# Optimization experiments

Measured on AMD Instinct MI355X. Metric: run time of the kernel, lower is better.

## Reference

```python
import jax, jax.numpy as jnp
import numpy as np

LN_EPS = 1e-5

def _layernorm(x, g, b):
    mu = jnp.mean(x, axis=-1, keepdims=True)
    var = jnp.mean((x - mu) ** 2, axis=-1, keepdims=True)
    return (x - mu) * jax.lax.rsqrt(var + LN_EPS) * g + b

def _mlp(x, w0, b0, wh, bh, lng, lnb, wout, bout):
    # Linear -> ReLU -> LN, repeated; final Linear.
    h = _layernorm(jax.nn.relu(x @ w0.T + b0), lng[0], lnb[0])
    for i in range(wh.shape[0]):
        h = _layernorm(jax.nn.relu(h @ wh[i].T + bh[i]), lng[i + 1], lnb[i + 1])
    return h @ wout.T + bout

def _vq(z, codebook, commitment_cost=0.25):
    B, A, D = z.shape
    flat = z.reshape(-1, D)                                  # [N, D]
    d = (jnp.sum(flat ** 2, axis=1, keepdims=True)
         + jnp.sum(codebook ** 2, axis=1)
         - 2.0 * flat @ codebook.T)                          # [N, K]
    idx = jnp.argmin(d, axis=1)                              # [N]
    quantized = codebook[idx].reshape(z.shape)               # gather, not one-hot matmul
    e_latent = jnp.mean((jax.lax.stop_gradient(quantized) - z) ** 2)
    q_latent = jnp.mean((quantized - jax.lax.stop_gradient(z)) ** 2)
    vq_loss = commitment_cost * e_latent + q_latent
    quantized = z + jax.lax.stop_gradient(quantized - z)     # straight-through
    return quantized, vq_loss

def setup_inputs() -> dict:
    key = jax.random.key(0)
    ks = jax.random.split(key, 8)
    H, D, K = 256, 64, 512
    B, A = 2048, 128
    s = lambda fan_in: 1.0 / np.sqrt(fan_in)
    return {
        'x': jax.random.normal(ks[0], (B, A, 3), jnp.float32),
        'enc_w0': jax.random.normal(ks[1], (H, 3), jnp.float32) * s(3),
        'enc_b0': jnp.zeros((H,), jnp.float32),
        'enc_wh': jax.random.normal(ks[2], (2, H, H), jnp.float32) * s(H),
        'enc_bh': jnp.zeros((2, H), jnp.float32),
        'enc_ln_g': jnp.ones((3, H), jnp.float32),
        'enc_ln_b': jnp.zeros((3, H), jnp.float32),
        'enc_wout': jax.random.normal(ks[3], (D, H), jnp.float32) * s(H),
        'enc_bout': jnp.zeros((D,), jnp.float32),
        'codebook': jax.random.uniform(ks[4], (K, D), jnp.float32, -1.0 / K, 1.0 / K),
        'dec_w0': jax.random.normal(ks[5], (H, D), jnp.float32) * s(D),
        'dec_b0': jnp.zeros((H,), jnp.float32),
        'dec_wh': jax.random.normal(ks[6], (2, H, H), jnp.float32) * s(H),
        'dec_bh': jnp.zeros((2, H), jnp.float32),
        'dec_ln_g': jnp.ones((3, H), jnp.float32),
        'dec_ln_b': jnp.zeros((3, H), jnp.float32),
        'dec_wout': jax.random.normal(ks[7], (3, H), jnp.float32) * s(H),
        'dec_bout': jnp.zeros((3,), jnp.float32),
    }

def reference(x, enc_w0, enc_b0, enc_wh, enc_bh, enc_ln_g, enc_ln_b, enc_wout, enc_bout,
              codebook, dec_w0, dec_b0, dec_wh, dec_bh, dec_ln_g, dec_ln_b, dec_wout, dec_bout):
    z = _mlp(x, enc_w0, enc_b0, enc_wh, enc_bh, enc_ln_g, enc_ln_b, enc_wout, enc_bout)
    quantized, vq_loss = _vq(z, codebook)
    recon = _mlp(quantized, dec_w0, dec_b0, dec_wh, dec_bh, dec_ln_g, dec_ln_b, dec_wout, dec_bout)
    loss = jnp.mean((recon - x) ** 2) + vq_loss
    return recon, quantized, loss
```

## Files before the change

### kernel.cpp

```cpp
#include <hip/hip_runtime.h>
#include <math.h>

__device__ __forceinline__ float fma4(float4 w, float4 a, float acc) {
  return fmaf(w.w, a.w, fmaf(w.z, a.z, fmaf(w.y, a.y, fmaf(w.x, a.x, acc))));
}


template <int NKQ>
__device__ __forceinline__ void gemmW(const float (*A)[256], const float* __restrict__ WT,
                                      float* acc, int r0, int c0) {
  #pragma unroll
  for (int i = 0; i < 32; ++i) acc[i] = 0.f;
  #pragma unroll 1
  for (int kq = 0; kq < NKQ; ++kq) {
    float4 wv[8];
    #pragma unroll
    for (int kk = 0; kk < 4; ++kk) {
      wv[kk * 2]     = *(const float4*)&WT[(size_t)(kq * 4 + kk) * 256 + c0];
      wv[kk * 2 + 1] = *(const float4*)&WT[(size_t)(kq * 4 + kk) * 256 + c0 + 4];
    }
    float4 a_[4];
    #pragma unroll
    for (int i = 0; i < 4; ++i) a_[i] = *(const float4*)&A[r0 + i][kq * 4];
    #pragma unroll
    for (int kk = 0; kk < 4; ++kk) {
      const float4 wlo = wv[kk * 2], whi = wv[kk * 2 + 1];
      #pragma unroll
      for (int i = 0; i < 4; ++i) {
        const float av = kk == 0 ? a_[i].x : kk == 1 ? a_[i].y : kk == 2 ? a_[i].z : a_[i].w;
        acc[i * 8 + 0] = fmaf(av, wlo.x, acc[i * 8 + 0]);
        acc[i * 8 + 1] = fmaf(av, wlo.y, acc[i * 8 + 1]);
        acc[i * 8 + 2] = fmaf(av, wlo.z, acc[i * 8 + 2]);
        acc[i * 8 + 3] = fmaf(av, wlo.w, acc[i * 8 + 3]);
        acc[i * 8 + 4] = fmaf(av, whi.x, acc[i * 8 + 4]);
        acc[i * 8 + 5] = fmaf(av, whi.y, acc[i * 8 + 5]);
        acc[i * 8 + 6] = fmaf(av, whi.z, acc[i * 8 + 6]);
        acc[i * 8 + 7] = fmaf(av, whi.w, acc[i * 8 + 7]);
      }
    }
  }
}

__device__ __forceinline__ void bias_relu(float* acc, const float* __restrict__ Bp, int c0) {
  float bv[8];
  *(float4*)&bv[0] = *(const float4*)&Bp[c0];
  *(float4*)&bv[4] = *(const float4*)&Bp[c0 + 4];
  #pragma unroll
  for (int rr = 0; rr < 4; ++rr)
    #pragma unroll
    for (int c = 0; c < 8; ++c)
      acc[rr * 8 + c] = fmaxf(acc[rr * 8 + c] + bv[c], 0.f);
}

__device__ __forceinline__ void ln16(float* acc, float* P36,
                                     const float* __restrict__ gg,
                                     const float* __restrict__ bb,
                                     int t, int r0, int c0) {
  const int slot = ((t >> 6) << 4) | (t & 15);
  float mu[4];
  __syncthreads();
  #pragma unroll
  for (int rr = 0; rr < 4; ++rr) {
    const float* a = &acc[rr * 8];
    P36[(r0 + rr) * 36 + slot] =
        (((a[0] + a[1]) + (a[2] + a[3])) + ((a[4] + a[5]) + (a[6] + a[7])));
  }
  __syncthreads();
  if (t < 16) {
    float q[8];
    #pragma unroll
    for (int j = 0; j < 8; ++j) {
      const float4 u = *(const float4*)&P36[t * 36 + 4 * j];
      q[j] = (u.x + u.y) + (u.z + u.w);
    }
    const float s = ((q[0] + q[1]) + (q[2] + q[3])) + ((q[4] + q[5]) + (q[6] + q[7]));
    P36[t * 36 + 32] = s * (1.f / 256.f);
  }
  __syncthreads();
  #pragma unroll
  for (int rr = 0; rr < 4; ++rr) mu[rr] = P36[(r0 + rr) * 36 + 32];
  __syncthreads();
  #pragma unroll
  for (int rr = 0; rr < 4; ++rr) {
    const float* a = &acc[rr * 8];
    const float m = mu[rr];
    const float d0 = a[0] - m, d1 = a[1] - m, d2 = a[2] - m, d3 = a[3] - m;
    const float d4 = a[4] - m, d5 = a[5] - m, d6 = a[6] - m, d7 = a[7] - m;
    float s = d0 * d0;
    s = fmaf(d1, d1, s); s = fmaf(d2, d2, s); s = fmaf(d3, d3, s);
    s = fmaf(d4, d4, s); s = fmaf(d5, d5, s); s = fmaf(d6, d6, s); s = fmaf(d7, d7, s);
    P36[(r0 + rr) * 36 + slot] = s;
  }
  __syncthreads();
  if (t < 16) {
    float q[8];
    #pragma unroll
    for (int j = 0; j < 8; ++j) {
      const float4 u = *(const float4*)&P36[t * 36 + 4 * j];
      q[j] = (u.x + u.y) + (u.z + u.w);
    }
    const float s2 = ((q[0] + q[1]) + (q[2] + q[3])) + ((q[4] + q[5]) + (q[6] + q[7]));
    P36[t * 36 + 32] = 1.f / sqrtf(s2 * (1.f / 256.f) + 1e-5f);
  }
  __syncthreads();
  float gv[8], bv[8];
  *(float4*)&gv[0] = *(const float4*)&gg[c0];
  *(float4*)&gv[4] = *(const float4*)&gg[c0 + 4];
  *(float4*)&bv[0] = *(const float4*)&bb[c0];
  *(float4*)&bv[4] = *(const float4*)&bb[c0 + 4];
  #pragma unroll
  for (int rr = 0; rr < 4; ++rr) {
    const float rs = P36[(r0 + rr) * 36 + 32];
    const float m = mu[rr];
    #pragma unroll
    for (int c = 0; c < 8; ++c)
      acc[rr * 8 + c] = ((acc[rr * 8 + c] - m) * rs) * gv[c] + bv[c];
  }
}

__device__ __forceinline__ void storeA16(float (*A)[256], const float* acc, int r0, int c0) {
  #pragma unroll
  for (int rr = 0; rr < 4; ++rr) {
    *(float4*)&A[r0 + rr][c0] =
        make_float4(acc[rr * 8], acc[rr * 8 + 1], acc[rr * 8 + 2], acc[rr * 8 + 3]);
    *(float4*)&A[r0 + rr][c0 + 4] =
        make_float4(acc[rr * 8 + 4], acc[rr * 8 + 5], acc[rr * 8 + 6], acc[rr * 8 + 7]);
  }
}

__global__ __launch_bounds__(128, 4) void k_mlp(
    const float* __restrict__ x, const float* __restrict__ w0, const float* __restrict__ b0,
    const float* __restrict__ wt1, const float* __restrict__ wt2, const float* __restrict__ bh,
    const float* __restrict__ lng, const float* __restrict__ lnb,
    const float* __restrict__ wtout, const float* __restrict__ bout, float* __restrict__ z,
    const float* __restrict__ cb, const float* __restrict__ wt0d, const float* __restrict__ db0,
    const float* __restrict__ wtd1, const float* __restrict__ wtd2, const float* __restrict__ dbh,
    const float* __restrict__ dlng, const float* __restrict__ dlnb,
    const float* __restrict__ dwout, const float* __restrict__ dbout,
    float* __restrict__ table, float* __restrict__ ne) {
  __shared__ float A[16][256];
  float* Pa = &A[0][0];
  const int t = threadIdx.x;
  const int w = t >> 6;
  const int li = t & 15;
  const int g = (t >> 4) & 3;
  const int c0 = w * 128 + li * 8;
  const int r0 = g * 4;
  float acc[32];

  if (blockIdx.x >= 32) {
    const size_t rbase = (size_t)(blockIdx.x - 32) * 16;
    {
      float wv[24], bv[8];
      #pragma unroll
      for (int i = 0; i < 6; ++i) *(float4*)&wv[i * 4] = *(const float4*)&w0[c0 * 3 + i * 4];
      *(float4*)&bv[0] = *(const float4*)&b0[c0];
      *(float4*)&bv[4] = *(const float4*)&b0[c0 + 4];
      #pragma unroll
      for (int rr = 0; rr < 4; ++rr) {
        const size_t r3 = (rbase + r0 + rr) * 3;
        const float x0 = x[r3], x1 = x[r3 + 1], x2 = x[r3 + 2];
        #pragma unroll
        for (int c = 0; c < 8; ++c) {
          const float s = fmaf(wv[c * 3 + 2], x2, fmaf(wv[c * 3 + 1], x1, wv[c * 3] * x0));
          acc[rr * 8 + c] = fmaxf(s + bv[c], 0.f);
        }
      }
    }
    ln16(acc, Pa, lng, lnb, t, r0, c0);
    __syncthreads();
    storeA16(A, acc, r0, c0);
    __syncthreads();

    gemmW<64>(A, wt1, acc, r0, c0);
    bias_relu(acc, bh, c0);
    ln16(acc, Pa, lng + 256, lnb + 256, t, r0, c0);
    __syncthreads();
    storeA16(A, acc, r0, c0);
    __syncthreads();

    gemmW<64>(A, wt2, acc, r0, c0);
    bias_relu(acc, bh + 256, c0);
    ln16(acc, Pa, lng + 512, lnb + 512, t, r0, c0);
    __syncthreads();
    storeA16(A, acc, r0, c0);
    __syncthreads();

    {
      const int l6 = t & 63;
      const int col = w * 32 + (l6 & 31);
      const int rg8 = (l6 >> 5) * 8;
      float o[8];
      #pragma unroll
      for (int i = 0; i < 8; ++i) o[i] = 0.f;
      #pragma unroll 1
      for (int kq = 0; kq < 64; ++kq) {
        float4 a_[8];
        #pragma unroll
        for (int i = 0; i < 8; ++i) a_[i] = *(const float4*)&A[rg8 + i][kq * 4];
        #pragma unroll
        for (int kk = 0; kk < 4; ++kk) {
          const float wv = wtout[(size_t)(kq * 4 + kk) * 64 + col];
          #pragma unroll
          for (int i = 0; i < 8; ++i) {
            const float av = kk == 0 ? a_[i].x : kk == 1 ? a_[i].y : kk == 2 ? a_[i].z : a_[i].w;
            o[i] = fmaf(av, wv, o[i]);
          }
        }
      }
      const float bb = bout[col];
      #pragma unroll
      for (int rr = 0; rr < 8; ++rr)
        z[(rbase + rg8 + rr) * 64 + col] = o[rr] + bb;
    }
  } else {
    const int cbase = blockIdx.x * 16;
    if (t < 16) {
      float s = 0.f;
      #pragma unroll 8
      for (int k = 0; k < 64; ++k) {
        const float v = cb[(size_t)(cbase + t) * 64 + k];
        s = fmaf(v, v, s);
      }
      ne[cbase + t] = s;
    }
    {
      const float4* cbf = (const float4*)(cb + (size_t)cbase * 64);
      #pragma unroll
      for (int i = 0; i < 2; ++i) {
        const int j = t * 2 + i;
        *(float4*)&A[j >> 4][(j & 15) * 4] = cbf[j];
      }
    }
    __syncthreads();

    gemmW<16>(A, wt0d, acc, r0, c0);
    bias_relu(acc, db0, c0);
    ln16(acc, Pa, dlng, dlnb, t, r0, c0);
    __syncthreads();
    storeA16(A, acc, r0, c0);
    __syncthreads();

    gemmW<64>(A, wtd1, acc, r0, c0);
    bias_relu(acc, dbh, c0);
    ln16(acc, Pa, dlng + 256, dlnb + 256, t, r0, c0);
    __syncthreads();
    storeA16(A, acc, r0, c0);
    __syncthreads();

    gemmW<64>(A, wtd2, acc, r0, c0);
    bias_relu(acc, dbh + 256, c0);
    ln16(acc, Pa, dlng + 512, dlnb + 512, t, r0, c0);
    __syncthreads();
    storeA16(A, acc, r0, c0);
    __syncthreads();

    if (t < 16) {
      #pragma unroll
      for (int j = 0; j < 3; ++j) {
        float s = 0.f;
        #pragma unroll 4
        for (int kq = 0; kq < 64; ++kq) {
          const float4 wq = *(const float4*)&dwout[j * 256 + kq * 4];
          const float4 a = *(const float4*)&A[t][kq * 4];
          s = fma4(wq, a, s);
        }
        table[(cbase + t) * 3 + j] = s + dbout[j];
      }
    }
  }
}

__global__ __launch_bounds__(256) void k_wt(
    const float* __restrict__ wh, const float* __restrict__ wout,
    const float* __restrict__ dwh, const float* __restrict__ dw0,
    float* __restrict__ wt1, float* __restrict__ wt2, float* __restrict__ wtout,
    float* __restrict__ wtd1, float* __restrict__ wtd2, float* __restrict__ wt0d) {
  const int b = blockIdx.x, t = threadIdx.x;
  if (b < 256) {
    wt1[b * 256 + t] = wh[t * 256 + b];
  } else if (b < 512) {
    const int k = b - 256;
    wt2[k * 256 + t] = wh[65536 + t * 256 + k];
  } else if (b < 576) {
    const int k = (b - 512) * 4 + (t >> 6);
    const int j = t & 63;
    wtout[k * 64 + j] = wout[j * 256 + k];
  } else if (b < 832) {
    const int k = b - 576;
    wtd1[k * 256 + t] = dwh[t * 256 + k];
  } else if (b < 1088) {
    const int k = b - 832;
    wtd2[k * 256 + t] = dwh[65536 + t * 256 + k];
  } else {
    const int k = b - 1088;
    wt0d[k * 256 + t] = dw0[t * 64 + k];
  }
}

__global__ __launch_bounds__(256) void k_vq(
    float* __restrict__ zq_io, const float* __restrict__ cb,
    const float* __restrict__ ne, const float* __restrict__ table,
    const float* __restrict__ x, float* __restrict__ recon,
    float* __restrict__ psr, float* __restrict__ psv) {
  __shared__ float red[256];
  const int t = threadIdx.x;
  const int row = blockIdx.x * 256 + t;
  float4 zf[16];
  {
    const float4* zp = (const float4*)(zq_io + (size_t)row * 64);
    #pragma unroll
    for (int q = 0; q < 16; ++q) zf[q] = zp[q];
  }
  float nz = 0.f;
  #pragma unroll
  for (int q = 0; q < 16; ++q) {
    nz = fmaf(zf[q].x, zf[q].x, nz);
    nz = fmaf(zf[q].y, zf[q].y, nz);
    nz = fmaf(zf[q].z, zf[q].z, nz);
    nz = fmaf(zf[q].w, zf[q].w, nz);
  }
  float dmin = INFINITY; int imin = 0;
  const float4* cbv = (const float4*)cb;
  for (int c = 0; c < 512; ++c) {
    float da = 0.f, db = 0.f;
    #pragma unroll
    for (int q = 0; q < 16; q += 2) {
      const float4 ea = cbv[c * 16 + q];
      const float4 eb = cbv[c * 16 + q + 1];
      da = fmaf(ea.x, zf[q].x, da);
      da = fmaf(ea.y, zf[q].y, da);
      da = fmaf(ea.z, zf[q].z, da);
      da = fmaf(ea.w, zf[q].w, da);
      db = fmaf(eb.x, zf[q + 1].x, db);
      db = fmaf(eb.y, zf[q + 1].y, db);
      db = fmaf(eb.z, zf[q + 1].z, db);
      db = fmaf(eb.w, zf[q + 1].w, db);
    }
    const float dot = da + db;
    const float d = (nz + ne[c]) - 2.f * dot;
    if (d < dmin) { dmin = d; imin = c; }
  }
  float sv = 0.f;
  {
    const float4* eq = (const float4*)(cb + imin * 64);
    float4* qo = (float4*)(zq_io + (size_t)row * 64);
    #pragma unroll
    for (int q = 0; q < 16; ++q) {
      const float4 e = eq[q];
      const float4 zz = zf[q];
      const float ax = e.x - zz.x, ay = e.y - zz.y, az = e.z - zz.z, aw = e.w - zz.w;
      sv = fmaf(ax, ax, sv); sv = fmaf(ay, ay, sv);
      sv = fmaf(az, az, sv); sv = fmaf(aw, aw, sv);
      float4 st;
      st.x = zz.x + ax; st.y = zz.y + ay; st.z = zz.z + az; st.w = zz.w + aw;
      qo[q] = st;
    }
  }
  const float r0 = table[imin * 3], r1 = table[imin * 3 + 1], r2 = table[imin * 3 + 2];
  recon[row * 3] = r0; recon[row * 3 + 1] = r1; recon[row * 3 + 2] = r2;
  const float e0 = r0 - x[row * 3], e1 = r1 - x[row * 3 + 1], e2 = r2 - x[row * 3 + 2];
  const float sr = fmaf(e2, e2, fmaf(e1, e1, e0 * e0));
  red[t] = sr; __syncthreads();
  #pragma unroll
  for (int o = 128; o > 0; o >>= 1) { if (t < o) red[t] += red[t + o]; __syncthreads(); }
  if (t == 0) psr[blockIdx.x] = red[0];
  __syncthreads();
  red[t] = sv; __syncthreads();
  #pragma unroll
  for (int o = 128; o > 0; o >>= 1) { if (t < o) red[t] += red[t + o]; __syncthreads(); }
  if (t == 0) psv[blockIdx.x] = red[0];
}

__global__ __launch_bounds__(256) void k_loss(
    const float* __restrict__ psr, const float* __restrict__ psv,
    float* __restrict__ out) {
  __shared__ float ra[256], rb[256];
  const int t = threadIdx.x;
  const float sr = ((psr[t] + psr[t + 256]) + psr[t + 512]) + psr[t + 768];
  const float sv = ((psv[t] + psv[t + 256]) + psv[t + 512]) + psv[t + 768];
  ra[t] = sr; rb[t] = sv;
  __syncthreads();
  #pragma unroll
  for (int o = 128; o > 0; o >>= 1) {
    if (t < o) { ra[t] += ra[t + o]; rb[t] += rb[t + o]; }
    __syncthreads();
  }
  if (t == 0) {
    const float mr = ra[0] / 786432.f;
    const float mv = rb[0] * (1.f / 16777216.f);
    const float vq = 0.25f * mv + mv;
    out[0] = mr + vq;
  }
}

extern "C" void kernel_launch(void* const* d_in, const int* in_sizes, int n_in,
                              void* d_out, int out_size, void* d_ws, size_t ws_size,
                              hipStream_t stream) {
  const float* x        = (const float*)d_in[0];
  const float* enc_w0   = (const float*)d_in[1];
  const float* enc_b0   = (const float*)d_in[2];
  const float* enc_wh   = (const float*)d_in[3];
  const float* enc_bh   = (const float*)d_in[4];
  const float* enc_lng  = (const float*)d_in[5];
  const float* enc_lnb  = (const float*)d_in[6];
  const float* enc_wout = (const float*)d_in[7];
  const float* enc_bout = (const float*)d_in[8];
  const float* cb       = (const float*)d_in[9];
  const float* dec_w0   = (const float*)d_in[10];
  const float* dec_b0   = (const float*)d_in[11];
  const float* dec_wh   = (const float*)d_in[12];
  const float* dec_bh   = (const float*)d_in[13];
  const float* dec_lng  = (const float*)d_in[14];
  const float* dec_lnb  = (const float*)d_in[15];
  const float* dec_wout = (const float*)d_in[16];
  const float* dec_bout = (const float*)d_in[17];

  float* out   = (float*)d_out;
  float* recon = out;
  float* qbuf  = out + 786432;
  float* lossp = out + 786432 + 16777216;

  float* wt1   = out;
  float* wt2   = out + 65536;
  float* wtout = out + 131072;
  float* wtd1  = out + 147456;
  float* wtd2  = out + 212992;
  float* wt0d  = out + 278528;

  float* ws    = (float*)d_ws;
  float* ne    = ws;
  float* table = ws + 512;
  float* psr   = ws + 2048;
  float* psv   = ws + 3072;

  k_wt<<<1152, 256, 0, stream>>>(enc_wh, enc_wout, dec_wh, dec_w0,
                                 wt1, wt2, wtout, wtd1, wtd2, wt0d);
  k_mlp<<<16416, 128, 0, stream>>>(x, enc_w0, enc_b0, wt1, wt2, enc_bh,
                                   enc_lng, enc_lnb, wtout, enc_bout, qbuf,
                                   cb, wt0d, dec_b0, wtd1, wtd2, dec_bh,
                                   dec_lng, dec_lnb, dec_wout, dec_bout,
                                   table, ne);
  k_vq<<<1024, 256, 0, stream>>>(qbuf, cb, ne, table, x, recon, psr, psv);
  k_loss<<<1, 256, 0, stream>>>(psr, psv, lossp);
}
```

Measured before the change: 1.455 ms.

## Double-buffer weight loads in MLP GEMM, pad shared rows, relax launch bounds

The inner GEMM loop now prefetches the next k-chunk of weights into a second register buffer while computing on the current one, so global load latency overlaps with FMAs. Shared activation rows are padded from 256 to 260 floats to reduce LDS bank conflicts. Launch bounds change from 4 to 2 minimum blocks per SM so the compiler can use more registers for the extra buffer. The cost is fewer resident waves, and any code that indexes A through the flat Pa pointer with a stride of 256 would now address the wrong elements.

```diff
diff --git a/kernel.cpp b/kernel.cpp
--- a/kernel.cpp
+++ b/kernel.cpp
@@ -6,36 +6,73 @@
 }
 
 
+#define ASTRIDE 260
+
 template <int NKQ>
-__device__ __forceinline__ void gemmW(const float (*A)[256], const float* __restrict__ WT,
+__device__ __forceinline__ void gemmW(const float (*A)[ASTRIDE], const float* __restrict__ WT,
                                       float* acc, int r0, int c0) {
   #pragma unroll
   for (int i = 0; i < 32; ++i) acc[i] = 0.f;
+  float4 wA[8], wB[8];
+  #pragma unroll
+  for (int kk = 0; kk < 4; ++kk) {
+    wA[kk * 2]     = *(const float4*)&WT[(size_t)kk * 256 + c0];
+    wA[kk * 2 + 1] = *(const float4*)&WT[(size_t)kk * 256 + c0 + 4];
+  }
   #pragma unroll 1
-  for (int kq = 0; kq < NKQ; ++kq) {
-    float4 wv[8];
+  for (int kq = 0; kq < NKQ; kq += 2) {
     #pragma unroll
     for (int kk = 0; kk < 4; ++kk) {
-      wv[kk * 2]     = *(const float4*)&WT[(size_t)(kq * 4 + kk) * 256 + c0];
-      wv[kk * 2 + 1] = *(const float4*)&WT[(size_t)(kq * 4 + kk) * 256 + c0 + 4];
-    }
-    float4 a_[4];
-    #pragma unroll
-    for (int i = 0; i < 4; ++i) a_[i] = *(const float4*)&A[r0 + i][kq * 4];
-    #pragma unroll
-    for (int kk = 0; kk < 4; ++kk) {
-      const float4 wlo = wv[kk * 2], whi = wv[kk * 2 + 1];
-      #pragma unroll
-      for (int i = 0; i < 4; ++i) {
-        const float av = kk == 0 ? a_[i].x : kk == 1 ? a_[i].y : kk == 2 ? a_[i].z : a_[i].w;
-        acc[i * 8 + 0] = fmaf(av, wlo.x, acc[i * 8 + 0]);
-        acc[i * 8 + 1] = fmaf(av, wlo.y, acc[i * 8 + 1]);
-        acc[i * 8 + 2] = fmaf(av, wlo.z, acc[i * 8 + 2]);
-        acc[i * 8 + 3] = fmaf(av, wlo.w, acc[i * 8 + 3]);
-        acc[i * 8 + 4] = fmaf(av, whi.x, acc[i * 8 + 4]);
-        acc[i * 8 + 5] = fmaf(av, whi.y, acc[i * 8 + 5]);
-        acc[i * 8 + 6] = fmaf(av, whi.z, acc[i * 8 + 6]);
-        acc[i * 8 + 7] = fmaf(av, whi.w, acc[i * 8 + 7]);
+      wB[kk * 2]     = *(const float4*)&WT[(size_t)((kq + 1) * 4 + kk) * 256 + c0];
+      wB[kk * 2 + 1] = *(const float4*)&WT[(size_t)((kq + 1) * 4 + kk) * 256 + c0 + 4];
+    }
+    {
+      float4 a_[4];
+      #pragma unroll
+      for (int i = 0; i < 4; ++i) a_[i] = *(const float4*)&A[r0 + i][kq * 4];
+      #pragma unroll
+      for (int kk = 0; kk < 4; ++kk) {
+        const float4 wlo = wA[kk * 2], whi = wA[kk * 2 + 1];
+        #pragma unroll
+        for (int i = 0; i < 4; ++i) {
+          const float av = kk == 0 ? a_[i].x : kk == 1 ? a_[i].y : kk == 2 ? a_[i].z : a_[i].w;
+          acc[i * 8 + 0] = fmaf(av, wlo.x, acc[i * 8 + 0]);
+          acc[i * 8 + 1] = fmaf(av, wlo.y, acc[i * 8 + 1]);
+          acc[i * 8 + 2] = fmaf(av, wlo.z, acc[i * 8 + 2]);
+          acc[i * 8 + 3] = fmaf(av, wlo.w, acc[i * 8 + 3]);
+          acc[i * 8 + 4] = fmaf(av, whi.x, acc[i * 8 + 4]);
+          acc[i * 8 + 5] = fmaf(av, whi.y, acc[i * 8 + 5]);
+          acc[i * 8 + 6] = fmaf(av, whi.z, acc[i * 8 + 6]);
+          acc[i * 8 + 7] = fmaf(av, whi.w, acc[i * 8 + 7]);
+        }
+      }
+    }
+    if (kq + 2 < NKQ) {
+      #pragma unroll
+      for (int kk = 0; kk < 4; ++kk) {
+        wA[kk * 2]     = *(const float4*)&WT[(size_t)((kq + 2) * 4 + kk) * 256 + c0];
+        wA[kk * 2 + 1] = *(const float4*)&WT[(size_t)((kq + 2) * 4 + kk) * 256 + c0 + 4];
+      }
+    }
+    {
+      float4 a_[4];
+      #pragma unroll
+      for (int i = 0; i < 4; ++i) a_[i] = *(const float4*)&A[r0 + i][(kq + 1) * 4];
+      #pragma unroll
+      for (int kk = 0; kk < 4; ++kk) {
+        const float4 wlo = wB[kk * 2], whi = wB[kk * 2 + 1];
+        #pragma unroll
+        for (int i = 0; i < 4; ++i) {
+          const float av = kk == 0 ? a_[i].x : kk == 1 ? a_[i].y : kk == 2 ? a_[i].z : a_[i].w;
+          acc[i * 8 + 0] = fmaf(av, wlo.x, acc[i * 8 + 0]);
+          acc[i * 8 + 1] = fmaf(av, wlo.y, acc[i * 8 + 1]);
+          acc[i * 8 + 2] = fmaf(av, wlo.z, acc[i * 8 + 2]);
+          acc[i * 8 + 3] = fmaf(av, wlo.w, acc[i * 8 + 3]);
+          acc[i * 8 + 4] = fmaf(av, whi.x, acc[i * 8 + 4]);
+          acc[i * 8 + 5] = fmaf(av, whi.y, acc[i * 8 + 5]);
+          acc[i * 8 + 6] = fmaf(av, whi.z, acc[i * 8 + 6]);
+          acc[i * 8 + 7] = fmaf(av, whi.w, acc[i * 8 + 7]);
+        }
       }
     }
   }
@@ -118,7 +155,7 @@
   }
 }
 
-__device__ __forceinline__ void storeA16(float (*A)[256], const float* acc, int r0, int c0) {
+__device__ __forceinline__ void storeA16(float (*A)[ASTRIDE], const float* acc, int r0, int c0) {
   #pragma unroll
   for (int rr = 0; rr < 4; ++rr) {
     *(float4*)&A[r0 + rr][c0] =
@@ -128,7 +165,7 @@
   }
 }
 
-__global__ __launch_bounds__(128, 4) void k_mlp(
+__global__ __launch_bounds__(128, 2) void k_mlp(
     const float* __restrict__ x, const float* __restrict__ w0, const float* __restrict__ b0,
     const float* __restrict__ wt1, const float* __restrict__ wt2, const float* __restrict__ bh,
     const float* __restrict__ lng, const float* __restrict__ lnb,
@@ -138,7 +175,7 @@
     const float* __restrict__ dlng, const float* __restrict__ dlnb,
     const float* __restrict__ dwout, const float* __restrict__ dbout,
     float* __restrict__ table, float* __restrict__ ne) {
-  __shared__ float A[16][256];
+  __shared__ float A[16][ASTRIDE];
   float* Pa = &A[0][0];
   const int t = threadIdx.x;
   const int w = t >> 6;
```

New measurement: 1.518 ms. 1.04x slower.
